# Kernel tuning notes

Measured on AMD Instinct MI355X. Metric: run time of the kernel, lower is better.

The kernel has to match this reference:

```python
import jax, jax.numpy as jnp
import numpy as np

NUM_CAPSULE = 10
DIM_CAPSULE = 16
ROUTINGS = 3
EPS = 1e-7  # K.epsilon()


def squash(x, axis=-1):
    # bojone squash: x / sqrt(s2 + eps) * s2 / (1 + s2)
    s2 = jnp.sum(jnp.square(x), axis=axis, keepdims=True)
    return x * s2 / ((1.0 + s2) * jnp.sqrt(s2 + EPS))


def setup_inputs() -> dict:
    key = jax.random.key(0)
    k1, k2 = jax.random.split(key)
    B, N, D_in = 64, 2048, 128  # batch, input_num_capsule, input_dim_capsule
    u_vecs = jax.random.normal(k1, (B, N, D_in), dtype=jnp.float32)
    fan_out = NUM_CAPSULE * DIM_CAPSULE
    limit = float(np.sqrt(6.0 / (D_in + fan_out)))  # glorot_uniform
    W = jax.random.uniform(k2, (D_in, fan_out), dtype=jnp.float32,
                           minval=-limit, maxval=limit)
    return {"u_vecs": u_vecs, "W": W}


def reference(u_vecs, W):
    B, N, _ = u_vecs.shape
    # share_weights=True: conv1d with kernel size 1 == matmul over feature dim
    u_hat = (u_vecs @ W).reshape(B, N, NUM_CAPSULE, DIM_CAPSULE)
    u_hat = jnp.transpose(u_hat, (0, 2, 1, 3))  # (B, J, N, D)
    b = jnp.zeros((B, NUM_CAPSULE, N), dtype=u_vecs.dtype)
    o = jnp.zeros((B, NUM_CAPSULE, DIM_CAPSULE), dtype=u_vecs.dtype)
    for i in range(ROUTINGS):
        c = jax.nn.softmax(b, axis=1)           # softmax over output capsules
        o = jnp.einsum('bjn,bjnd->bjd', c, u_hat)
        if i < ROUTINGS - 1:
            b = jnp.einsum('bjd,bjnd->bjn', o, u_hat)  # agreement update
    return squash(o)
```

## Files before the change

kernel.cpp:

```cpp
#include <hip/hip_runtime.h>
#include <math.h>


#define BATCH 64
#define NN    2048
#define KD    128
#define JCAP  10
#define DCAP  16
#define JDIM  160
#define EPSQ  1e-7f
#define NT    32
#define TROW  64

#define WS_OP 0
#define WS_V  (BATCH * NT * JDIM)

__device__ __forceinline__ void gload16(const float* g, float4* l) {
  __builtin_amdgcn_global_load_lds(
      (const __attribute__((address_space(1))) void*)g,
      (__attribute__((address_space(3))) void*)l, 16, 0, 0);
}

__global__ __launch_bounds__(256) void f_iter0(const float* __restrict__ u,
                                               const float* __restrict__ W,
                                               float* __restrict__ Op) {
  const int b = blockIdx.y, tile = blockIdx.x, t = threadIdx.x;
  __shared__ __align__(16) float4 red[256];
  __shared__ float S_s[KD];
  const int c = t & 31, rg = t >> 5;
  const float* p = u + (((size_t)(b * NN + tile * TROW + rg * 8)) << 7) + (c << 2);
  float4 a = make_float4(0.f, 0.f, 0.f, 0.f);
#pragma unroll
  for (int r = 0; r < 8; ++r) {
    const float4 w4 = *(const float4*)(p + ((size_t)r << 7));
    a.x += w4.x; a.y += w4.y; a.z += w4.z; a.w += w4.w;
  }
  red[t] = a;
  __syncthreads();
  if (t < 32) {
    float4 s4 = red[t];
#pragma unroll
    for (int g = 1; g < 8; ++g) {
      const float4 w4 = red[g * 32 + t];
      s4.x += w4.x; s4.y += w4.y; s4.z += w4.z; s4.w += w4.w;
    }
    s4.x *= 0.1f; s4.y *= 0.1f; s4.z *= 0.1f; s4.w *= 0.1f;
    *(float4*)&S_s[t * 4] = s4;
  }
  __syncthreads();
  if (t < JDIM) {
    float acc = 0.f;
#pragma unroll 4
    for (int k = 0; k < KD; ++k) acc += S_s[k] * W[k * JDIM + t];
    Op[((size_t)(b * NT) + tile) * JDIM + t] = acc;
  }
}

__global__ __launch_bounds__(128) void f_makeV(const float* __restrict__ Op,
                                               const float* __restrict__ W,
                                               float* __restrict__ V) {
  const int j = blockIdx.x, b = blockIdx.y, t = threadIdx.x;
  __shared__ float o_s[DCAP];
  if (t < DCAP) {
    float s = 0.f;
    const float* p = Op + (size_t)b * NT * JDIM + j * DCAP + t;
#pragma unroll
    for (int tl = 0; tl < NT; ++tl) s += p[tl * JDIM];
    o_s[t] = s;
  }
  __syncthreads();
  const float* wp = W + t * JDIM + j * DCAP;
  float acc = 0.f;
#pragma unroll
  for (int d = 0; d < DCAP; ++d) acc += wp[d] * o_s[d];
  V[((size_t)(b * JCAP + j) << 7) + t] = acc;
}

__global__ __launch_bounds__(256) void f_route(const float* __restrict__ u,
                                               const float* __restrict__ V,
                                               const float* __restrict__ W,
                                               float* __restrict__ Op) {
  const int b = blockIdx.y, tile = blockIdx.x, t = threadIdx.x;
  const int r0 = tile * TROW;
  __shared__ __align__(16) float4 u4[TROW * 32];
  __shared__ __align__(16) float Cs[JCAP][TROW];
  __shared__ __align__(16) float Gp[4 * JCAP * KD];

  {
    const float* ub = u + (((size_t)(b * NN + r0)) << 7);
    const int wbase = t & 192;
#pragma unroll
    for (int p = 0; p < 8; ++p) {
      const int s = p * 256 + t;
      const int r = s >> 5, csl = s & 31;
      const int c = csl ^ (r & 7);
      gload16(ub + (((size_t)r) << 7) + (c << 2), &u4[p * 256 + wbase]);
    }
  }
  __syncthreads();

  {
    const int r = t & 63;
    const int q = __builtin_amdgcn_readfirstlane(t >> 6);
    const float* vb = V + (((size_t)(b * JCAP)) << 7) + (q << 5);
    float acc[JCAP];
#pragma unroll
    for (int j = 0; j < JCAP; ++j) acc[j] = 0.f;
#pragma unroll
    for (int c4 = 0; c4 < 8; ++c4) {
      const float4 uu = u4[(r << 5) + ((q * 8 + c4) ^ (r & 7))];
#pragma unroll
      for (int j = 0; j < JCAP; ++j) {
        const float4 vv = *(const float4*)(vb + (j << 7) + (c4 << 2));
        acc[j] += uu.x * vv.x + uu.y * vv.y + uu.z * vv.z + uu.w * vv.w;
      }
    }
    float* Pl = Gp;
#pragma unroll
    for (int j = 0; j < JCAP; ++j) Pl[(q * JCAP + j) * 64 + r] = acc[j];
  }
  __syncthreads();
  if (t < TROW) {
    const float* Pl = Gp;
    float lg[JCAP];
    float m = -1e30f;
#pragma unroll
    for (int j = 0; j < JCAP; ++j) {
      const float s = Pl[j * 64 + t] + Pl[(JCAP + j) * 64 + t]
                    + Pl[(2 * JCAP + j) * 64 + t] + Pl[(3 * JCAP + j) * 64 + t];
      lg[j] = s; m = fmaxf(m, s);
    }
    float ssum = 0.f;
#pragma unroll
    for (int j = 0; j < JCAP; ++j) { lg[j] = __expf(lg[j] - m); ssum += lg[j]; }
    const float inv = 1.f / ssum;
#pragma unroll
    for (int j = 0; j < JCAP; ++j) Cs[j][t] = lg[j] * inv;
  }
  __syncthreads();

  {
    const int w = t >> 6, lane = t & 63;
    const int rw = w * 16;
    const int chalf = lane >> 1, cin = (lane & 1) << 1;
    float g0[JCAP], g1[JCAP];
#pragma unroll
    for (int j = 0; j < JCAP; ++j) { g0[j] = 0.f; g1[j] = 0.f; }
    for (int rc = 0; rc < 16; rc += 4) {
      float ua[4], uc[4];
#pragma unroll
      for (int qq = 0; qq < 4; ++qq) {
        const int r = rw + rc + qq;
        const float2 uu2 =
            *(const float2*)((const float*)&u4[(r << 5) + (chalf ^ (r & 7))] + cin);
        ua[qq] = uu2.x; uc[qq] = uu2.y;
      }
#pragma unroll
      for (int j = 0; j < JCAP; ++j) {
        const float4 c4v = *(const float4*)&Cs[j][rw + rc];
        g0[j] += c4v.x * ua[0] + c4v.y * ua[1] + c4v.z * ua[2] + c4v.w * ua[3];
        g1[j] += c4v.x * uc[0] + c4v.y * uc[1] + c4v.z * uc[2] + c4v.w * uc[3];
      }
    }
#pragma unroll
    for (int j = 0; j < JCAP; ++j)
      *(float2*)&Gp[(w * JCAP + j) * KD + 2 * lane] = make_float2(g0[j], g1[j]);
  }
  __syncthreads();
  for (int i = t; i < JCAP * KD; i += 256)
    Gp[i] += Gp[JCAP * KD + i] + Gp[2 * JCAP * KD + i] + Gp[3 * JCAP * KD + i];
  __syncthreads();
  if (t < JDIM) {
    const int j = t >> 4;
    const float* gj = Gp + j * KD;
    float acc = 0.f;
#pragma unroll 4
    for (int kk = 0; kk < KD; ++kk) {
      const int k = (kk + 3 * j) & 127;
      acc += gj[k] * W[k * JDIM + t];
    }
    Op[((size_t)(b * NT) + tile) * JDIM + t] = acc;
  }
}

__global__ __launch_bounds__(192) void f_squash(const float* __restrict__ Op,
                                                float* __restrict__ out) {
  const int b = blockIdx.x, t = threadIdx.x;
  __shared__ float o_s[JDIM];
  __shared__ float sc[JCAP];
  if (t < JDIM) {
    float s = 0.f;
    const float* p = Op + (size_t)b * NT * JDIM + t;
#pragma unroll
    for (int tl = 0; tl < NT; ++tl) s += p[tl * JDIM];
    o_s[t] = s;
  }
  __syncthreads();
  if (t < JCAP) {
    float s2 = 0.f;
#pragma unroll
    for (int d = 0; d < DCAP; ++d) { const float x = o_s[t * DCAP + d]; s2 += x * x; }
    sc[t] = s2 / ((1.f + s2) * sqrtf(s2 + EPSQ));
  }
  __syncthreads();
  if (t < JDIM) out[b * JDIM + t] = o_s[t] * sc[t >> 4];
}

extern "C" void kernel_launch(void* const* d_in, const int* in_sizes, int n_in,
                              void* d_out, int out_size, void* d_ws, size_t ws_size,
                              hipStream_t stream) {
  const float* u = (const float*)d_in[0];
  const float* W = (const float*)d_in[1];
  float* out = (float*)d_out;
  float* ws  = (float*)d_ws;

  float* Op = ws + WS_OP;
  float* V  = ws + WS_V;
  f_iter0 <<<dim3(NT, BATCH), 256, 0, stream>>>(u, W, Op);
  f_makeV <<<dim3(JCAP, BATCH), 128, 0, stream>>>(Op, W, V);
  f_route <<<dim3(NT, BATCH), 256, 0, stream>>>(u, V, W, Op);
  f_makeV <<<dim3(JCAP, BATCH), 128, 0, stream>>>(Op, W, V);
  f_route <<<dim3(NT, BATCH), 256, 0, stream>>>(u, V, W, Op);
  f_squash<<<BATCH, 192, 0, stream>>>(Op, out);
}
```

Measured before the change: 201.7 us.

## Halve routing tile rows, stage V in LDS, split capsules across waves

Rows per tile drop from 64 to 32, which doubles the grid to 64 tiles per batch and shrinks shared memory per block, aiming for more blocks in flight. V is now copied into LDS with async global-to-LDS loads instead of being read from global memory in the dot-product loop. The partial logits are combined with a wave shuffle. In the weighted-sum stage each wave now owns a subset of capsules across all rows, which removes the 4-way partial-sum reduction and one barrier. The trade-off is twice as many Op partials for makeV and squash to sum, and uneven work per wave (3,3,2,2 capsules).

```diff
diff --git a/kernel.cpp b/kernel.cpp
--- a/kernel.cpp
+++ b/kernel.cpp
@@ -9,13 +9,14 @@
 #define DCAP  16
 #define JDIM  160
 #define EPSQ  1e-7f
-#define NT    32
-#define TROW  64
+#define NT    64
+#define TROW  32
+#define GSTR  132
 
 #define WS_OP 0
 #define WS_V  (BATCH * NT * JDIM)
 
-__device__ __forceinline__ void gload16(const float* g, float4* l) {
+__device__ __forceinline__ void gload16(const float* g, void* l) {
   __builtin_amdgcn_global_load_lds(
       (const __attribute__((address_space(1))) void*)g,
       (__attribute__((address_space(3))) void*)l, 16, 0, 0);
@@ -28,10 +29,10 @@
   __shared__ __align__(16) float4 red[256];
   __shared__ float S_s[KD];
   const int c = t & 31, rg = t >> 5;
-  const float* p = u + (((size_t)(b * NN + tile * TROW + rg * 8)) << 7) + (c << 2);
+  const float* p = u + (((size_t)(b * NN + tile * TROW + rg * 4)) << 7) + (c << 2);
   float4 a = make_float4(0.f, 0.f, 0.f, 0.f);
 #pragma unroll
-  for (int r = 0; r < 8; ++r) {
+  for (int r = 0; r < 4; ++r) {
     const float4 w4 = *(const float4*)(p + ((size_t)r << 7));
     a.x += w4.x; a.y += w4.y; a.z += w4.z; a.w += w4.w;
   }
@@ -83,51 +84,57 @@
   const int b = blockIdx.y, tile = blockIdx.x, t = threadIdx.x;
   const int r0 = tile * TROW;
   __shared__ __align__(16) float4 u4[TROW * 32];
+  __shared__ __align__(16) float4 Vs4[JCAP * 32];
   __shared__ __align__(16) float Cs[JCAP][TROW];
-  __shared__ __align__(16) float Gp[4 * JCAP * KD];
+  __shared__ __align__(16) float GpPl[JCAP * GSTR];
 
   {
     const float* ub = u + (((size_t)(b * NN + r0)) << 7);
     const int wbase = t & 192;
 #pragma unroll
-    for (int p = 0; p < 8; ++p) {
+    for (int p = 0; p < 4; ++p) {
       const int s = p * 256 + t;
       const int r = s >> 5, csl = s & 31;
       const int c = csl ^ (r & 7);
       gload16(ub + (((size_t)r) << 7) + (c << 2), &u4[p * 256 + wbase]);
     }
+    const float* vb = V + (((size_t)(b * JCAP)) << 7);
+    gload16(vb + (t << 2), &Vs4[wbase]);
+    if (t < 64) gload16(vb + ((256 + t) << 2), &Vs4[256]);
   }
   __syncthreads();
 
   {
-    const int r = t & 63;
-    const int q = __builtin_amdgcn_readfirstlane(t >> 6);
-    const float* vb = V + (((size_t)(b * JCAP)) << 7) + (q << 5);
+    const int r = t & 31, q8 = t >> 5;
     float acc[JCAP];
 #pragma unroll
     for (int j = 0; j < JCAP; ++j) acc[j] = 0.f;
 #pragma unroll
-    for (int c4 = 0; c4 < 8; ++c4) {
-      const float4 uu = u4[(r << 5) + ((q * 8 + c4) ^ (r & 7))];
+    for (int c4 = 0; c4 < 4; ++c4) {
+      const float4 uu = u4[(r << 5) + ((q8 * 4 + c4) ^ (r & 7))];
 #pragma unroll
       for (int j = 0; j < JCAP; ++j) {
-        const float4 vv = *(const float4*)(vb + (j << 7) + (c4 << 2));
+        const float4 vv = Vs4[j * 32 + q8 * 4 + c4];
         acc[j] += uu.x * vv.x + uu.y * vv.y + uu.z * vv.z + uu.w * vv.w;
       }
     }
-    float* Pl = Gp;
-#pragma unroll
-    for (int j = 0; j < JCAP; ++j) Pl[(q * JCAP + j) * 64 + r] = acc[j];
+#pragma unroll
+    for (int j = 0; j < JCAP; ++j) acc[j] += __shfl_xor(acc[j], 32, 64);
+    if ((t & 32) == 0) {
+      const int q4 = t >> 6;
+#pragma unroll
+      for (int j = 0; j < JCAP; ++j) GpPl[(q4 * JCAP + j) * TROW + r] = acc[j];
+    }
   }
   __syncthreads();
   if (t < TROW) {
-    const float* Pl = Gp;
     float lg[JCAP];
     float m = -1e30f;
 #pragma unroll
     for (int j = 0; j < JCAP; ++j) {
-      const float s = Pl[j * 64 + t] + Pl[(JCAP + j) * 64 + t]
-                    + Pl[(2 * JCAP + j) * 64 + t] + Pl[(3 * JCAP + j) * 64 + t];
+      const float s = GpPl[j * TROW + t] + GpPl[(JCAP + j) * TROW + t]
+                    + GpPl[(2 * JCAP + j) * TROW + t]
+                    + GpPl[(3 * JCAP + j) * TROW + t];
       lg[j] = s; m = fmaxf(m, s);
     }
     float ssum = 0.f;
@@ -140,45 +147,43 @@
   __syncthreads();
 
   {
-    const int w = t >> 6, lane = t & 63;
-    const int rw = w * 16;
-    const int chalf = lane >> 1, cin = (lane & 1) << 1;
-    float g0[JCAP], g1[JCAP];
-#pragma unroll
-    for (int j = 0; j < JCAP; ++j) { g0[j] = 0.f; g1[j] = 0.f; }
-    for (int rc = 0; rc < 16; rc += 4) {
+    const int w = t >> 6, l = t & 63;
+    const int j0 = (w < 2) ? 3 * w : 2 * w + 2;
+    const int jn = (w < 2) ? 3 : 2;
+    const int chalf = l >> 1, cin = (l & 1) << 1;
+    float g0[3], g1[3];
+#pragma unroll
+    for (int jj = 0; jj < 3; ++jj) { g0[jj] = 0.f; g1[jj] = 0.f; }
+    for (int rc = 0; rc < TROW; rc += 4) {
       float ua[4], uc[4];
 #pragma unroll
       for (int qq = 0; qq < 4; ++qq) {
-        const int r = rw + rc + qq;
+        const int r = rc + qq;
         const float2 uu2 =
             *(const float2*)((const float*)&u4[(r << 5) + (chalf ^ (r & 7))] + cin);
         ua[qq] = uu2.x; uc[qq] = uu2.y;
       }
 #pragma unroll
-      for (int j = 0; j < JCAP; ++j) {
-        const float4 c4v = *(const float4*)&Cs[j][rw + rc];
-        g0[j] += c4v.x * ua[0] + c4v.y * ua[1] + c4v.z * ua[2] + c4v.w * ua[3];
-        g1[j] += c4v.x * uc[0] + c4v.y * uc[1] + c4v.z * uc[2] + c4v.w * uc[3];
+      for (int jj = 0; jj < 3; ++jj) {
+        if (jj < jn) {
+          const float4 c4v = *(const float4*)&Cs[j0 + jj][rc];
+          g0[jj] += c4v.x * ua[0] + c4v.y * ua[1] + c4v.z * ua[2] + c4v.w * ua[3];
+          g1[jj] += c4v.x * uc[0] + c4v.y * uc[1] + c4v.z * uc[2] + c4v.w * uc[3];
+        }
       }
     }
 #pragma unroll
-    for (int j = 0; j < JCAP; ++j)
-      *(float2*)&Gp[(w * JCAP + j) * KD + 2 * lane] = make_float2(g0[j], g1[j]);
-  }
-  __syncthreads();
-  for (int i = t; i < JCAP * KD; i += 256)
-    Gp[i] += Gp[JCAP * KD + i] + Gp[2 * JCAP * KD + i] + Gp[3 * JCAP * KD + i];
+    for (int jj = 0; jj < 3; ++jj)
+      if (jj < jn)
+        *(float2*)&GpPl[(j0 + jj) * GSTR + 2 * l] = make_float2(g0[jj], g1[jj]);
+  }
   __syncthreads();
   if (t < JDIM) {
     const int j = t >> 4;
-    const float* gj = Gp + j * KD;
+    const float* gj = GpPl + j * GSTR;
     float acc = 0.f;
 #pragma unroll 4
-    for (int kk = 0; kk < KD; ++kk) {
-      const int k = (kk + 3 * j) & 127;
-      acc += gj[k] * W[k * JDIM + t];
-    }
+    for (int k = 0; k < KD; ++k) acc += gj[k] * W[k * JDIM + t];
     Op[((size_t)(b * NT) + tile) * JDIM + t] = acc;
   }
 }
```

Result: faster. 180.9 us (-10.3%).
